# Kernel optimization log

Hardware: AMD Instinct MI355X
Metric: run time of the kernel (lower is better)

Reference implementation:

```python
import jax, jax.numpy as jnp
import numpy as np
from functools import partial

NUM_ITERS = 3
NUM_CAPS = 8      # primary capsule count
NUM_CLASSES = 10
OUT_CH = 16       # digit capsule dim
INPUT_SIZE = 32 * 6 * 6  # 1152 primary capsule units per capsule map


def squash(s, axis=-1):
    # faithful to non_linear_squashing: s * (||s||^2/(1+||s||^2)) / (||s||+1e-10)
    norm_sqr = jnp.sum(s * s, axis=axis, keepdims=True)
    scale = jnp.sqrt(norm_sqr) + 1e-10
    mag = norm_sqr / (1.0 + norm_sqr)
    return s * mag / scale


def conv2d(x, w, b, stride):
    y = jax.lax.conv_general_dilated(
        x, w, window_strides=(stride, stride), padding='VALID',
        dimension_numbers=('NCHW', 'OIHW', 'NCHW'))
    return y + b[None, :, None, None]


def setup_inputs() -> dict:
    key = jax.random.key(0)
    ks = jax.random.split(key, 6)
    B = 256
    x = jax.random.normal(ks[0], (B, 1, 28, 28), dtype=jnp.float32)
    conv_w = jax.random.normal(ks[1], (256, 1, 9, 9), dtype=jnp.float32) * 0.05
    conv_b = jax.random.normal(ks[2], (256,), dtype=jnp.float32) * 0.05
    # 8 primary capsule conv units (256->32 each) fused into one 256->256 conv
    prim_w = jax.random.normal(ks[3], (NUM_CAPS * 32, 256, 9, 9), dtype=jnp.float32) * 0.02
    prim_b = jax.random.normal(ks[4], (NUM_CAPS * 32,), dtype=jnp.float32) * 0.02
    # digit routing weights (input_size, num_classes, out_channels, num_capsules)
    digit_w = jax.random.normal(ks[5], (INPUT_SIZE, NUM_CLASSES, OUT_CH, NUM_CAPS), dtype=jnp.float32)
    return {'x': x, 'conv_w': conv_w, 'conv_b': conv_b,
            'prim_w': prim_w, 'prim_b': prim_b, 'digit_w': digit_w}


def reference(x, conv_w, conv_b, prim_w, prim_b, digit_w):
    B = x.shape[0]
    # conv stack: 1->256 k9 s1 + ReLU  (28 -> 20); pool is MaxPool2d(1,1) = identity
    h = jax.nn.relu(conv2d(x, conv_w, conv_b, stride=1))  # (B,256,20,20)
    # primary capsules: 8 convs 256->32 k9 s2, no activation (nl_activation=False)
    p = conv2d(h, prim_w, prim_b, stride=2)               # (B,256,6,6)
    u = p.reshape(B, NUM_CAPS, -1)                        # (B,8,1152)
    u = squash(u, axis=-1)
    # digit layer with dynamic routing
    # u_i: (B, IS, 8);  u_j_i[b,i,c,o] = sum_k W[i,c,o,k] * u_i[b,i,k]
    u_i = jnp.transpose(u, (0, 2, 1))                     # (B,1152,8)
    u_j_i = jnp.einsum('icok,bik->bico', digit_w, u_i)    # (B,1152,10,16)
    b_ij = jnp.zeros((INPUT_SIZE, NUM_CLASSES), dtype=x.dtype)
    out = None
    for _ in range(NUM_ITERS):
        c_ij = jax.nn.softmax(b_ij, axis=0)               # softmax over input capsules (dim=1 in torch)
        s_j = jnp.einsum('ic,bico->bco', c_ij, u_j_i)     # (B,10,16)
        # original squashes (B,1,C,16,1) along dim=2 == the CLASS axis
        out = squash(s_j, axis=1)                         # (B,10,16)
        # agreement: mean over batch of <u_j_i, v_j>
        u_v = jnp.einsum('bico,bco->ic', u_j_i, out) / B  # (1152,10)
        b_ij = b_ij + u_v
    # torch returns out.squeeze(1) with shape (B, C, 16, 1)
    return out[..., None]
```

## Files before the change

### kernel.cpp

```cpp
#include <hip/hip_runtime.h>
#include <cstdint>
#include <cstddef>


typedef __attribute__((ext_vector_type(8))) short short8;
typedef __attribute__((ext_vector_type(4))) float f32x4;

#define PHALF 2359296

__device__ __forceinline__ unsigned short f2bf_rn(float x) {
    unsigned u = __float_as_uint(x);
    unsigned r = (u + 0x7fffu + ((u >> 16) & 1u)) >> 16;
    return (unsigned short)r;
}

__global__ void k_pre(const float* __restrict__ x, const float* __restrict__ cw,
                      const float* __restrict__ cb, const float* __restrict__ w2,
                      unsigned short* __restrict__ h, unsigned short* __restrict__ wt) {
    __shared__ float sh[3376];
    int blk = blockIdx.x, t = threadIdx.x;
    if (blk < 2048) {
        float* img = sh;
        float* wsm = sh + 784;
        int b = blk >> 3, ocg = blk & 7;
        for (int idx = t; idx < 784; idx += 256) img[idx] = x[b * 784 + idx];
        for (int idx = t; idx < 2592; idx += 256) wsm[idx] = cw[ocg * 2592 + idx];
        __syncthreads();
        int oc_l = t & 31, g = t >> 5;
        int oc = ocg * 32 + oc_l;
        float bias = cb[oc];
        const float* wp = &wsm[oc_l * 81];
        for (int q = g; q < 100; q += 8) {
            int py = q / 5, qx = (q % 5) * 4;
            float a0 = bias, a1 = bias, a2 = bias, a3 = bias;
            #pragma unroll
            for (int ky = 0; ky < 9; ky++) {
                const float* ir = &img[(py + ky) * 28 + qx];
                float r[12];
                #pragma unroll
                for (int j = 0; j < 12; j++) r[j] = ir[j];
                #pragma unroll
                for (int kx = 0; kx < 9; kx++) {
                    float w = wp[ky * 9 + kx];
                    a0 += r[kx] * w; a1 += r[kx + 1] * w;
                    a2 += r[kx + 2] * w; a3 += r[kx + 3] * w;
                }
            }
            float v[4] = { fmaxf(a0, 0.f), fmaxf(a1, 0.f), fmaxf(a2, 0.f), fmaxf(a3, 0.f) };
            size_t base = ((size_t)b * 400 + py * 20 + qx) * 256 + oc;
            #pragma unroll
            for (int j = 0; j < 4; j++)
                h[base + (size_t)j * 256] = f2bf_rn(v[j]);
        }
    } else {
        int m2 = blk - 2048;
        int oc = m2 >> 3, icg = m2 & 7;
        float* lw2 = sh;
        for (int idx = t; idx < 2592; idx += 256) {
            int ic_l = idx / 81, k = idx % 81;
            lw2[idx] = w2[((size_t)oc * 256 + icg * 32 + ic_l) * 81 + k];
        }
        __syncthreads();
        for (int idx = t; idx < 324; idx += 256) {
            int k = idx >> 2, sl = idx & 3;
            unsigned short hi8[8];
            #pragma unroll
            for (int j = 0; j < 8; j++)
                hi8[j] = f2bf_rn(lw2[(sl * 8 + j) * 81 + k]);
            size_t o = ((size_t)(k * 256 + oc)) * 256 + icg * 32 + sl * 8;
            *(uint4*)&wt[o] = *(uint4*)hi8;
        }
    }
}

__global__ __launch_bounds__(256, 4) void k_conv2m(
    const unsigned short* __restrict__ h,
    const unsigned short* __restrict__ wt,
    float* __restrict__ p0, float* __restrict__ p1,
    float* __restrict__ p2, float* __restrict__ p3)
{
    __shared__ unsigned short smem[14336];
    const int t = threadIdx.x;
    const int w = t >> 6, l = t & 63;
    const int mb = blockIdx.x, nb = blockIdx.y, zz = blockIdx.z;
    const int half = zz >> 1, seg = zz & 1;

    const unsigned short* src;
    int nld, sbase;
    unsigned rowbase[8];
    if (w < 2) {
        src = h; nld = 6; sbase = w * 3072;
        #pragma unroll
        for (int ld = 0; ld < 6; ld++) {
            int row = w * 48 + ld * 8 + (l >> 3);
            int c = l & 7;
            int g = c ^ (row & 7);
            int P = mb * 96 + row;
            int b = P / 36, o = P % 36;
            int oy = o / 6, ox = o % 6;
            rowbase[ld] = (unsigned)((b * 400 + oy * 40 + ox * 2) * 256 + half * 128 + g * 8);
        }
    } else {
        src = wt; nld = 8; sbase = 6144 + (w - 2) * 4096;
        #pragma unroll
        for (int ld = 0; ld < 8; ld++) {
            int oc = (w - 2) * 64 + ld * 8 + (l >> 3);
            int c = l & 7;
            int g = c ^ (oc & 7);
            rowbase[ld] = (unsigned)((nb * 128 + oc) * 256 + half * 128 + g * 8);
        }
    }

    const int wm = w & 1, wn = w >> 1;
    const int lane16 = l & 15, q = l >> 4;

    f32x4 acc[3][4] = {};

    const int pos0 = seg ? 41 : 0;
    const int pos1 = seg ? 81 : 41;
    for (int pos = pos0; pos < pos1; ++pos) {
        const int ky = pos / 9, kx = pos - ky * 9;
        const unsigned kbase = (w < 2) ? (unsigned)((ky * 20 + kx) * 256)
                                       : (unsigned)(pos * 65536);
        for (int icc = 0; icc < 2; ++icc) {
            const unsigned kofs = kbase + icc * 64;
            __syncthreads();
            for (int ld = 0; ld < nld; ld++) {
                __builtin_amdgcn_global_load_lds(
                    (const __attribute__((address_space(1))) unsigned int*)(const void*)(src + rowbase[ld] + kofs),
                    (__attribute__((address_space(3))) unsigned int*)(void*)(smem + sbase + ld * 512),
                    16, 0, 0);
            }
            __syncthreads();
            #pragma unroll
            for (int ic2 = 0; ic2 < 2; ic2++) {
                short8 a[3], b[4];
                #pragma unroll
                for (int mt = 0; mt < 3; mt++) {
                    int pixL = wm * 48 + mt * 16 + lane16;
                    int ps = (ic2 * 4 + q) ^ (pixL & 7);
                    a[mt] = *(const short8*)(smem + pixL * 64 + ps * 8);
                }
                #pragma unroll
                for (int nt = 0; nt < 4; nt++) {
                    int ocL = wn * 64 + nt * 16 + lane16;
                    int ps = (ic2 * 4 + q) ^ (ocL & 7);
                    b[nt] = *(const short8*)(smem + 6144 + ocL * 64 + ps * 8);
                }
                #pragma unroll
                for (int mt = 0; mt < 3; mt++)
                    #pragma unroll
                    for (int nt = 0; nt < 4; nt++)
                        acc[mt][nt] = __builtin_amdgcn_mfma_f32_16x16x32_bf16(a[mt], b[nt], acc[mt][nt], 0, 0, 0);
            }
        }
    }

    #pragma unroll
    for (int mt = 0; mt < 3; mt++) {
        int pixG = mb * 96 + wm * 48 + mt * 16 + q * 4;
        int b = pixG / 36, p36 = pixG % 36;
        #pragma unroll
        for (int nt = 0; nt < 4; nt++) {
            int oc = nb * 128 + wn * 64 + nt * 16 + lane16;
            float* pout = (zz == 0) ? p0 : (zz == 1) ? p1 : (zz == 2) ? p2 : p3;
            *(f32x4*)&pout[((size_t)(b * 256 + oc)) * 36 + p36] = acc[mt][nt];
        }
    }
}

__global__ void k_squash1(const float* __restrict__ q0, const float* __restrict__ q1,
                          const float* __restrict__ q2, const float* __restrict__ q3,
                          const float* __restrict__ prim_b, float* __restrict__ U) {
    __shared__ float red[4];
    int b = blockIdx.x >> 3, cap = blockIdx.x & 7;
    int t = threadIdx.x;
    size_t base = ((size_t)b * 256 + cap * 32) * 36;
    const float* pa = q0 + base;
    const float* pb = q1 + base;
    const float* pc = q2 + base;
    const float* pd = q3 + base;
    float v[5];
    float ss = 0.f;
    #pragma unroll
    for (int j = 0; j < 5; j++) {
        int idx = t + j * 256;
        if (idx < 1152) {
            int ch_l = idx / 36;
            float val = pa[idx] + pb[idx] + pc[idx] + pd[idx] + prim_b[cap * 32 + ch_l];
            v[j] = val; ss += val * val;
        } else v[j] = 0.f;
    }
    for (int off = 32; off; off >>= 1) ss += __shfl_down(ss, off);
    if ((t & 63) == 0) red[t >> 6] = ss;
    __syncthreads();
    float n2 = red[0] + red[1] + red[2] + red[3];
    float f = (n2 / (1.0f + n2)) / (sqrtf(n2) + 1e-10f);
    #pragma unroll
    for (int j = 0; j < 5; j++) {
        int idx = t + j * 256;
        if (idx < 1152) U[(size_t)b * 9216 + idx * 8 + cap] = v[j] * f;
    }
}

__global__ void k_dwt2(const float* __restrict__ dw, float* __restrict__ dwT2) {
    int co = blockIdx.x, t = threadIdx.x;
    int c = co >> 4, o = co & 15;
    const float* base = dw + c * 128 + o * 8;
    float* out = dwT2 + (size_t)co * 9216;
    for (int idx = t; idx < 9216; idx += 256) {
        int i = idx >> 3, k = idx & 7;
        out[idx] = base[(size_t)i * 1280 + k];
    }
}

__global__ void k_softmax(const float* __restrict__ bij, float* __restrict__ csm) {
    __shared__ float red[4];
    int c = blockIdx.x, t = threadIdx.x;
    float vals[5];
    float mx = -1e30f;
    #pragma unroll
    for (int j = 0; j < 5; j++) {
        int i = t + j * 256;
        vals[j] = (i < 1152) ? bij[i * 10 + c] : -1e30f;
        mx = fmaxf(mx, vals[j]);
    }
    for (int off = 32; off; off >>= 1) mx = fmaxf(mx, __shfl_down(mx, off));
    if ((t & 63) == 0) red[t >> 6] = mx;
    __syncthreads();
    mx = fmaxf(fmaxf(red[0], red[1]), fmaxf(red[2], red[3]));
    __syncthreads();
    float s = 0.f;
    #pragma unroll
    for (int j = 0; j < 5; j++) {
        int i = t + j * 256;
        vals[j] = (i < 1152) ? expf(vals[j] - mx) : 0.f;
        s += vals[j];
    }
    for (int off = 32; off; off >>= 1) s += __shfl_down(s, off);
    if ((t & 63) == 0) red[t >> 6] = s;
    __syncthreads();
    s = red[0] + red[1] + red[2] + red[3];
    float inv = 1.0f / s;
    #pragma unroll
    for (int j = 0; j < 5; j++) {
        int i = t + j * 256;
        if (i < 1152) csm[i * 10 + c] = vals[j] * inv;
    }
}

__global__ __launch_bounds__(256) void k_gemm1(const float* __restrict__ U,
                                               const float* __restrict__ dwT2,
                                               const float* __restrict__ csm,
                                               float* __restrict__ part,
                                               int uniform) {
    __shared__ float Us[32 * 36];
    __shared__ float WsT[5120];
    __shared__ float cl[360];
    int mb = blockIdx.x, kc = blockIdx.y, t = threadIdx.x;
    int tc = t & 15, tb = t >> 4;
    if (!uniform)
        for (int idx = t; idx < 360; idx += 256) cl[idx] = csm[kc * 360 + idx];
    const float uscale = 1.0f / 1152.0f;
    float acc[2][10] = {};
    for (int ks = 0; ks < 9; ks++) {
        __syncthreads();
        {
            int bb = t >> 3, k4 = t & 7;
            *(float4*)&Us[bb * 36 + k4 * 4] =
                *(const float4*)&U[(size_t)(mb * 32 + bb) * 9216 + kc * 288 + ks * 32 + k4 * 4];
        }
        #pragma unroll
        for (int pass = 0; pass < 5; pass++) {
            int s = t + pass * 256;
            int co = s >> 3, p = s & 7;
            int kq = p ^ (co & 7);
            int ikl = ks * 32 + kq * 4;
            float4 v = *(const float4*)&dwT2[(size_t)co * 9216 + kc * 288 + ikl];
            float sc = uniform ? uscale : cl[(ikl >> 3) * 10 + (co >> 4)];
            v.x *= sc; v.y *= sc; v.z *= sc; v.w *= sc;
            *(float4*)&WsT[s * 4] = v;
        }
        __syncthreads();
        float a0[32], a1[32];
        #pragma unroll
        for (int kq = 0; kq < 8; kq++) {
            float4 v0 = *(const float4*)&Us[(tb * 2) * 36 + kq * 4];
            float4 v1 = *(const float4*)&Us[(tb * 2 + 1) * 36 + kq * 4];
            a0[kq * 4 + 0] = v0.x; a0[kq * 4 + 1] = v0.y; a0[kq * 4 + 2] = v0.z; a0[kq * 4 + 3] = v0.w;
            a1[kq * 4 + 0] = v1.x; a1[kq * 4 + 1] = v1.y; a1[kq * 4 + 2] = v1.z; a1[kq * 4 + 3] = v1.w;
        }
        #pragma unroll
        for (int j = 0; j < 10; j++) {
            int co = tc + 16 * j;
            int cx = co & 7, cbase = co * 32;
            #pragma unroll
            for (int kq = 0; kq < 8; kq++) {
                float4 wv = *(const float4*)&WsT[cbase + ((kq ^ cx) << 2)];
                acc[0][j] += a0[kq * 4 + 0] * wv.x; acc[0][j] += a0[kq * 4 + 1] * wv.y;
                acc[0][j] += a0[kq * 4 + 2] * wv.z; acc[0][j] += a0[kq * 4 + 3] * wv.w;
                acc[1][j] += a1[kq * 4 + 0] * wv.x; acc[1][j] += a1[kq * 4 + 1] * wv.y;
                acc[1][j] += a1[kq * 4 + 2] * wv.z; acc[1][j] += a1[kq * 4 + 3] * wv.w;
            }
        }
    }
    #pragma unroll
    for (int r = 0; r < 2; r++)
        #pragma unroll
        for (int j = 0; j < 10; j++)
            part[(size_t)kc * 40960 + (mb * 32 + tb * 2 + r) * 160 + tc + 16 * j] = acc[r][j];
}

__global__ void k_redsq(const float* __restrict__ part, float* __restrict__ out,
                        float* __restrict__ outT, int writeT) {
    __shared__ float sl[160];
    __shared__ float n2s[16];
    int b = blockIdx.x, t = threadIdx.x;
    float s = 0.f;
    if (t < 160) {
        for (int kc = 0; kc < 32; kc++) s += part[(size_t)kc * 40960 + b * 160 + t];
        sl[t] = s;
    }
    __syncthreads();
    if (t < 16) {
        float n2 = 0.f;
        #pragma unroll
        for (int c = 0; c < 10; c++) { float v = sl[c * 16 + t]; n2 += v * v; }
        n2s[t] = n2;
    }
    __syncthreads();
    if (t < 160) {
        float n2 = n2s[t & 15];
        float f = (n2 / (1.0f + n2)) / (sqrtf(n2) + 1e-10f);
        float r = s * f;
        out[(size_t)b * 160 + t] = r;
        if (writeT) outT[(size_t)t * 256 + b] = r;
    }
}

__global__ __launch_bounds__(256) void k_g2uv(const float* __restrict__ U,
                                              const float* __restrict__ outTg,
                                              const float* __restrict__ dw,
                                              float* __restrict__ bij) {
    __shared__ float UsT[1024];
    __shared__ float OsT[5120];
    __shared__ float dwl[5120];
    __shared__ float sb[320];
    int blk = blockIdx.x, t = threadIdx.x;
    int tc = t & 15, tm = t >> 4;
    for (int idx = t; idx < 5120; idx += 256)
        dwl[idx] = dw[(size_t)blk * 5120 + idx];
    float acc[2][10] = {};
    for (int bs = 0; bs < 256; bs += 32) {
        __syncthreads();
        {
            int r = t >> 3, c4 = t & 7;
            float4 v = *(const float4*)&U[(size_t)(bs + r) * 9216 + blk * 32 + c4 * 4];
            int hi = ((r >> 2)) , lo = (r & 3);
            int m0 = c4 * 4;
            UsT[(m0 + 0) * 32 + ((hi ^ ((m0 + 0) & 7)) << 2) + lo] = v.x;
            UsT[(m0 + 1) * 32 + ((hi ^ ((m0 + 1) & 7)) << 2) + lo] = v.y;
            UsT[(m0 + 2) * 32 + ((hi ^ ((m0 + 2) & 7)) << 2) + lo] = v.z;
            UsT[(m0 + 3) * 32 + ((hi ^ ((m0 + 3) & 7)) << 2) + lo] = v.w;
        }
        #pragma unroll
        for (int pass = 0; pass < 5; pass++) {
            int s = t + pass * 256;
            int co = s >> 3, p = s & 7;
            int kq = p ^ (co & 7);
            *(float4*)&OsT[s * 4] =
                *(const float4*)&outTg[(size_t)co * 256 + bs + kq * 4];
        }
        __syncthreads();
        float a0[32], a1[32];
        int m0 = tm * 2, m1 = tm * 2 + 1;
        #pragma unroll
        for (int kq = 0; kq < 8; kq++) {
            float4 v0 = *(const float4*)&UsT[m0 * 32 + ((kq ^ (m0 & 7)) << 2)];
            float4 v1 = *(const float4*)&UsT[m1 * 32 + ((kq ^ (m1 & 7)) << 2)];
            a0[kq * 4 + 0] = v0.x; a0[kq * 4 + 1] = v0.y; a0[kq * 4 + 2] = v0.z; a0[kq * 4 + 3] = v0.w;
            a1[kq * 4 + 0] = v1.x; a1[kq * 4 + 1] = v1.y; a1[kq * 4 + 2] = v1.z; a1[kq * 4 + 3] = v1.w;
        }
        #pragma unroll
        for (int j = 0; j < 10; j++) {
            int co = tc + 16 * j;
            int cx = co & 7, cbase = co * 32;
            #pragma unroll
            for (int kq = 0; kq < 8; kq++) {
                float4 wv = *(const float4*)&OsT[cbase + ((kq ^ cx) << 2)];
                acc[0][j] += a0[kq * 4 + 0] * wv.x; acc[0][j] += a0[kq * 4 + 1] * wv.y;
                acc[0][j] += a0[kq * 4 + 2] * wv.z; acc[0][j] += a0[kq * 4 + 3] * wv.w;
                acc[1][j] += a1[kq * 4 + 0] * wv.x; acc[1][j] += a1[kq * 4 + 1] * wv.y;
                acc[1][j] += a1[kq * 4 + 2] * wv.z; acc[1][j] += a1[kq * 4 + 3] * wv.w;
            }
        }
    }
    #pragma unroll
    for (int r = 0; r < 2; r++) {
        int ik_l = tm * 2 + r;
        int i_l = ik_l >> 3, k = ik_l & 7;
        #pragma unroll
        for (int j = 0; j < 10; j++) {
            float v = acc[r][j] * dwl[i_l * 1280 + (j * 16 + tc) * 8 + k];
            v += __shfl_down(v, 8, 16);
            v += __shfl_down(v, 4, 16);
            v += __shfl_down(v, 2, 16);
            v += __shfl_down(v, 1, 16);
            if (tc == 0) sb[ik_l * 10 + j] = v;
        }
    }
    __syncthreads();
    if (t < 40) {
        int i_l = t / 10, c = t % 10;
        float s = 0.f;
        #pragma unroll
        for (int kk = 0; kk < 8; kk++) s += sb[(i_l * 8 + kk) * 10 + c];
        size_t o = (size_t)(blk * 4 + i_l) * 10 + c;
        bij[o] += s * (1.0f / 256.0f);
    }
}

extern "C" void kernel_launch(void* const* d_in, const int* in_sizes, int n_in,
                              void* d_out, int out_size, void* d_ws, size_t ws_size,
                              hipStream_t stream) {
    const float* x      = (const float*)d_in[0];
    const float* conv_w = (const float*)d_in[1];
    const float* conv_b = (const float*)d_in[2];
    const float* prim_w = (const float*)d_in[3];
    const float* prim_b = (const float*)d_in[4];
    const float* dw     = (const float*)d_in[5];

    char* wsb = (char*)d_ws;
    unsigned short* h  = (unsigned short*)(wsb);
    unsigned short* wt = (unsigned short*)(wsb + 52428800);
    float* pp0  = (float*)(wsb + 63045632);
    float* pp1  = (float*)(wsb + 72482816);
    float* U    = (float*)(wsb + 81920000);
    float* dwT2 = (float*)(wsb + 91357184);
    float* pp3  = (float*)(wsb + 91357184);
    float* part = (float*)(wsb + 97255424);
    float* csm  = (float*)(wsb + 102498304);
    float* bij  = (float*)(wsb + 102544384);
    float* outT = (float*)(wsb + 102590464);
    float* outw = (float*)(wsb + 102754304);
    float* pp2  = (float*)(wsb + 102918144);

    k_pre<<<4096, 256, 0, stream>>>(x, conv_w, conv_b, prim_w, h, wt);
    k_conv2m<<<dim3(96, 2, 4), 256, 0, stream>>>(h, wt, pp0, pp1, pp2, pp3);
    k_squash1<<<2048, 256, 0, stream>>>(pp0, pp1, pp2, pp3, prim_b, U);
    k_dwt2<<<160, 256, 0, stream>>>(dw, dwT2);
    hipMemsetAsync(bij, 0, 11520 * sizeof(float), stream);

    k_gemm1<<<dim3(8, 32), 256, 0, stream>>>(U, dwT2, csm, part, 1);
    k_redsq<<<256, 256, 0, stream>>>(part, outw, outT, 1);
    k_g2uv<<<288, 256, 0, stream>>>(U, outT, dw, bij);
    k_softmax<<<10, 256, 0, stream>>>(bij, csm);
    k_gemm1<<<dim3(8, 32), 256, 0, stream>>>(U, dwT2, csm, part, 0);
    k_redsq<<<256, 256, 0, stream>>>(part, outw, outT, 1);
    k_g2uv<<<288, 256, 0, stream>>>(U, outT, dw, bij);
    k_softmax<<<10, 256, 0, stream>>>(bij, csm);
    k_gemm1<<<dim3(8, 32), 256, 0, stream>>>(U, dwT2, csm, part, 0);
    k_redsq<<<256, 256, 0, stream>>>(part, (float*)d_out, outT, 0);
}
```

Measured before the change: 479.0 us.

## Fuse softmax into routing GEMM, merge squash with weight transpose, drop memset

The squash kernel and the digit-weight transpose now run as one launch split by block index. The separate softmax kernel is removed: each k_gemm1 block recomputes the full column softmax over bij redundantly and keeps only its own 36 rows. The memset of bij is replaced by a 'first' flag in k_g2uv that overwrites rather than accumulates. Together these cut several kernel launches and dependency bubbles, at the cost of 256 blocks each re-reading all of bij with ten serialized reductions.

```diff
diff --git a/kernel.cpp b/kernel.cpp
--- a/kernel.cpp
+++ b/kernel.cpp
@@ -169,98 +169,95 @@
     }
 }
 
-__global__ void k_squash1(const float* __restrict__ q0, const float* __restrict__ q1,
-                          const float* __restrict__ q2, const float* __restrict__ q3,
-                          const float* __restrict__ prim_b, float* __restrict__ U) {
+__global__ void k_sq1dw(const float* __restrict__ q0, const float* __restrict__ q1,
+                        const float* __restrict__ q2, const float* __restrict__ q3,
+                        const float* __restrict__ prim_b, float* __restrict__ U,
+                        const float* __restrict__ dw, float* __restrict__ dwT2) {
     __shared__ float red[4];
-    int b = blockIdx.x >> 3, cap = blockIdx.x & 7;
-    int t = threadIdx.x;
-    size_t base = ((size_t)b * 256 + cap * 32) * 36;
-    const float* pa = q0 + base;
-    const float* pb = q1 + base;
-    const float* pc = q2 + base;
-    const float* pd = q3 + base;
-    float v[5];
-    float ss = 0.f;
-    #pragma unroll
-    for (int j = 0; j < 5; j++) {
-        int idx = t + j * 256;
-        if (idx < 1152) {
-            int ch_l = idx / 36;
-            float val = pa[idx] + pb[idx] + pc[idx] + pd[idx] + prim_b[cap * 32 + ch_l];
-            v[j] = val; ss += val * val;
-        } else v[j] = 0.f;
-    }
-    for (int off = 32; off; off >>= 1) ss += __shfl_down(ss, off);
-    if ((t & 63) == 0) red[t >> 6] = ss;
-    __syncthreads();
-    float n2 = red[0] + red[1] + red[2] + red[3];
-    float f = (n2 / (1.0f + n2)) / (sqrtf(n2) + 1e-10f);
-    #pragma unroll
-    for (int j = 0; j < 5; j++) {
-        int idx = t + j * 256;
-        if (idx < 1152) U[(size_t)b * 9216 + idx * 8 + cap] = v[j] * f;
-    }
-}
-
-__global__ void k_dwt2(const float* __restrict__ dw, float* __restrict__ dwT2) {
-    int co = blockIdx.x, t = threadIdx.x;
-    int c = co >> 4, o = co & 15;
-    const float* base = dw + c * 128 + o * 8;
-    float* out = dwT2 + (size_t)co * 9216;
-    for (int idx = t; idx < 9216; idx += 256) {
-        int i = idx >> 3, k = idx & 7;
-        out[idx] = base[(size_t)i * 1280 + k];
-    }
-}
-
-__global__ void k_softmax(const float* __restrict__ bij, float* __restrict__ csm) {
-    __shared__ float red[4];
-    int c = blockIdx.x, t = threadIdx.x;
-    float vals[5];
-    float mx = -1e30f;
-    #pragma unroll
-    for (int j = 0; j < 5; j++) {
-        int i = t + j * 256;
-        vals[j] = (i < 1152) ? bij[i * 10 + c] : -1e30f;
-        mx = fmaxf(mx, vals[j]);
-    }
-    for (int off = 32; off; off >>= 1) mx = fmaxf(mx, __shfl_down(mx, off));
-    if ((t & 63) == 0) red[t >> 6] = mx;
-    __syncthreads();
-    mx = fmaxf(fmaxf(red[0], red[1]), fmaxf(red[2], red[3]));
-    __syncthreads();
-    float s = 0.f;
-    #pragma unroll
-    for (int j = 0; j < 5; j++) {
-        int i = t + j * 256;
-        vals[j] = (i < 1152) ? expf(vals[j] - mx) : 0.f;
-        s += vals[j];
-    }
-    for (int off = 32; off; off >>= 1) s += __shfl_down(s, off);
-    if ((t & 63) == 0) red[t >> 6] = s;
-    __syncthreads();
-    s = red[0] + red[1] + red[2] + red[3];
-    float inv = 1.0f / s;
-    #pragma unroll
-    for (int j = 0; j < 5; j++) {
-        int i = t + j * 256;
-        if (i < 1152) csm[i * 10 + c] = vals[j] * inv;
+    int blk = blockIdx.x, t = threadIdx.x;
+    if (blk < 2048) {
+        int b = blk >> 3, cap = blk & 7;
+        size_t base = ((size_t)b * 256 + cap * 32) * 36;
+        const float* pa = q0 + base;
+        const float* pb = q1 + base;
+        const float* pc = q2 + base;
+        const float* pd = q3 + base;
+        float v[5];
+        float ss = 0.f;
+        #pragma unroll
+        for (int j = 0; j < 5; j++) {
+            int idx = t + j * 256;
+            if (idx < 1152) {
+                int ch_l = idx / 36;
+                float val = pa[idx] + pb[idx] + pc[idx] + pd[idx] + prim_b[cap * 32 + ch_l];
+                v[j] = val; ss += val * val;
+            } else v[j] = 0.f;
+        }
+        for (int off = 32; off; off >>= 1) ss += __shfl_down(ss, off);
+        if ((t & 63) == 0) red[t >> 6] = ss;
+        __syncthreads();
+        float n2 = red[0] + red[1] + red[2] + red[3];
+        float f = (n2 / (1.0f + n2)) / (sqrtf(n2) + 1e-10f);
+        #pragma unroll
+        for (int j = 0; j < 5; j++) {
+            int idx = t + j * 256;
+            if (idx < 1152) U[(size_t)b * 9216 + idx * 8 + cap] = v[j] * f;
+        }
+    } else {
+        int co = blk - 2048;
+        int c = co >> 4, o = co & 15;
+        const float* base = dw + c * 128 + o * 8;
+        float* out = dwT2 + (size_t)co * 9216;
+        for (int idx = t; idx < 9216; idx += 256) {
+            int i = idx >> 3, k = idx & 7;
+            out[idx] = base[(size_t)i * 1280 + k];
+        }
     }
 }
 
 __global__ __launch_bounds__(256) void k_gemm1(const float* __restrict__ U,
                                                const float* __restrict__ dwT2,
-                                               const float* __restrict__ csm,
+                                               const float* __restrict__ bij,
                                                float* __restrict__ part,
                                                int uniform) {
     __shared__ float Us[32 * 36];
     __shared__ float WsT[5120];
     __shared__ float cl[360];
+    __shared__ float red[4];
     int mb = blockIdx.x, kc = blockIdx.y, t = threadIdx.x;
     int tc = t & 15, tb = t >> 4;
-    if (!uniform)
-        for (int idx = t; idx < 360; idx += 256) cl[idx] = csm[kc * 360 + idx];
+    if (!uniform) {
+        for (int c = 0; c < 10; ++c) {
+            float vals[5];
+            float mx = -1e30f;
+            #pragma unroll
+            for (int j = 0; j < 5; j++) {
+                int i = t + j * 256;
+                vals[j] = (i < 1152) ? bij[i * 10 + c] : -1e30f;
+                mx = fmaxf(mx, vals[j]);
+            }
+            for (int off = 32; off; off >>= 1) mx = fmaxf(mx, __shfl_down(mx, off));
+            if ((t & 63) == 0) red[t >> 6] = mx;
+            __syncthreads();
+            mx = fmaxf(fmaxf(red[0], red[1]), fmaxf(red[2], red[3]));
+            __syncthreads();
+            float s = 0.f;
+            #pragma unroll
+            for (int j = 0; j < 5; j++) {
+                int i = t + j * 256;
+                vals[j] = (i < 1152) ? expf(vals[j] - mx) : 0.f;
+                s += vals[j];
+            }
+            for (int off = 32; off; off >>= 1) s += __shfl_down(s, off);
+            if ((t & 63) == 0) red[t >> 6] = s;
+            __syncthreads();
+            s = red[0] + red[1] + red[2] + red[3];
+            float inv = 1.0f / s;
+            if (t < 36)
+                cl[t * 10 + c] = expf(bij[(kc * 36 + t) * 10 + c] - mx) * inv;
+            __syncthreads();
+        }
+    }
     const float uscale = 1.0f / 1152.0f;
     float acc[2][10] = {};
     for (int ks = 0; ks < 9; ks++) {
@@ -341,7 +338,8 @@
 __global__ __launch_bounds__(256) void k_g2uv(const float* __restrict__ U,
                                               const float* __restrict__ outTg,
                                               const float* __restrict__ dw,
-                                              float* __restrict__ bij) {
+                                              float* __restrict__ bij,
+                                              int first) {
     __shared__ float UsT[1024];
     __shared__ float OsT[5120];
     __shared__ float dwl[5120];
@@ -356,7 +354,7 @@
         {
             int r = t >> 3, c4 = t & 7;
             float4 v = *(const float4*)&U[(size_t)(bs + r) * 9216 + blk * 32 + c4 * 4];
-            int hi = ((r >> 2)) , lo = (r & 3);
+            int hi = (r >> 2), lo = (r & 3);
             int m0 = c4 * 4;
             UsT[(m0 + 0) * 32 + ((hi ^ ((m0 + 0) & 7)) << 2) + lo] = v.x;
             UsT[(m0 + 1) * 32 + ((hi ^ ((m0 + 1) & 7)) << 2) + lo] = v.y;
@@ -416,7 +414,8 @@
         #pragma unroll
         for (int kk = 0; kk < 8; kk++) s += sb[(i_l * 8 + kk) * 10 + c];
         size_t o = (size_t)(blk * 4 + i_l) * 10 + c;
-        bij[o] += s * (1.0f / 256.0f);
+        float v = s * (1.0f / 256.0f);
+        bij[o] = first ? v : (bij[o] + v);
     }
 }
 
@@ -432,14 +431,13 @@
 
     char* wsb = (char*)d_ws;
     unsigned short* h  = (unsigned short*)(wsb);
+    float* dwT2 = (float*)(wsb);
     unsigned short* wt = (unsigned short*)(wsb + 52428800);
     float* pp0  = (float*)(wsb + 63045632);
     float* pp1  = (float*)(wsb + 72482816);
     float* U    = (float*)(wsb + 81920000);
-    float* dwT2 = (float*)(wsb + 91357184);
     float* pp3  = (float*)(wsb + 91357184);
     float* part = (float*)(wsb + 97255424);
-    float* csm  = (float*)(wsb + 102498304);
     float* bij  = (float*)(wsb + 102544384);
     float* outT = (float*)(wsb + 102590464);
     float* outw = (float*)(wsb + 102754304);
@@ -447,18 +445,14 @@
 
     k_pre<<<4096, 256, 0, stream>>>(x, conv_w, conv_b, prim_w, h, wt);
     k_conv2m<<<dim3(96, 2, 4), 256, 0, stream>>>(h, wt, pp0, pp1, pp2, pp3);
-    k_squash1<<<2048, 256, 0, stream>>>(pp0, pp1, pp2, pp3, prim_b, U);
-    k_dwt2<<<160, 256, 0, stream>>>(dw, dwT2);
-    hipMemsetAsync(bij, 0, 11520 * sizeof(float), stream);
-
-    k_gemm1<<<dim3(8, 32), 256, 0, stream>>>(U, dwT2, csm, part, 1);
+    k_sq1dw<<<2208, 256, 0, stream>>>(pp0, pp1, pp2, pp3, prim_b, U, dw, dwT2);
+
+    k_gemm1<<<dim3(8, 32), 256, 0, stream>>>(U, dwT2, bij, part, 1);
     k_redsq<<<256, 256, 0, stream>>>(part, outw, outT, 1);
-    k_g2uv<<<288, 256, 0, stream>>>(U, outT, dw, bij);
-    k_softmax<<<10, 256, 0, stream>>>(bij, csm);
-    k_gemm1<<<dim3(8, 32), 256, 0, stream>>>(U, dwT2, csm, part, 0);
+    k_g2uv<<<288, 256, 0, stream>>>(U, outT, dw, bij, 1);
+    k_gemm1<<<dim3(8, 32), 256, 0, stream>>>(U, dwT2, bij, part, 0);
     k_redsq<<<256, 256, 0, stream>>>(part, outw, outT, 1);
-    k_g2uv<<<288, 256, 0, stream>>>(U, outT, dw, bij);
-    k_softmax<<<10, 256, 0, stream>>>(bij, csm);
-    k_gemm1<<<dim3(8, 32), 256, 0, stream>>>(U, dwT2, csm, part, 0);
+    k_g2uv<<<288, 256, 0, stream>>>(U, outT, dw, bij, 0);
+    k_gemm1<<<dim3(8, 32), 256, 0, stream>>>(U, dwT2, bij, part, 0);
     k_redsq<<<256, 256, 0, stream>>>(part, (float*)d_out, outT, 0);
 }
```

Result: slower. 490.1 us (+2.3%).
